# Performance work log

Measured on AMD Instinct MI355X. Metric: run time of the kernel, lower is better.

The kernel has to match this reference:

```python
import jax, jax.numpy as jnp
import numpy as np

B = 524288   # particles
H = 128      # hidden_size
E = 64       # embed_dim
NT = 512     # num trajectories
IN = 16 + 9 + E  # fc1 input dim = 89
EPS = 1e-6


def setup_inputs() -> dict:
    key = jax.random.key(0)
    ks = jax.random.split(key, 12)
    w = lambda k, shp, fan_in: (jax.random.normal(k, shp, dtype=jnp.float32)
                                / np.sqrt(fan_in).astype(np.float32))
    return {
        "F": jax.random.normal(ks[0], (B, 3, 3), dtype=jnp.float32),
        "C": jax.random.normal(ks[1], (B, 3, 3), dtype=jnp.float32),
        "traj_id": 7,
        "latent": jax.random.normal(ks[2], (NT, E), dtype=jnp.float32),
        "W1": w(ks[3], (IN, H), IN), "b1": jnp.zeros((H,), jnp.float32),
        "W2": w(ks[4], (H, H), H),   "b2": jnp.zeros((H,), jnp.float32),
        "W3": w(ks[5], (H, H), H),   "b3": jnp.zeros((H,), jnp.float32),
        "W4": w(ks[6], (H, H), H),   "b4": jnp.zeros((H,), jnp.float32),
        "W5": w(ks[7], (H, H), H),   "b5": jnp.zeros((H,), jnp.float32),
        "W6": w(ks[8], (H, H), H),   "b6": jnp.zeros((H,), jnp.float32),
        "W7": w(ks[9], (H, 9), H),   "b7": jnp.zeros((9,), jnp.float32),
    }


def _strain_features(F):
    # FFt: [B,3,3]; J = clamp(det F); J1 = clamp(F00); sigma: 3 singular values
    FFt = jnp.einsum('bij,bkj->bik', F, F)
    J = jnp.maximum(jnp.linalg.det(F), EPS)
    J1 = jnp.maximum(F[:, 0, 0], EPS)
    sigma = jnp.linalg.svd(F, compute_uv=False)  # descending, like torch.svd
    return jnp.concatenate([
        FFt.reshape(-1, 9),
        jnp.log(J)[:, None], sigma, J[:, None],
        jnp.log(J1)[:, None], J1[:, None],
    ], axis=-1)  # [B,16]


def reference(F, C, traj_id, latent,
              W1, b1, W2, b2, W3, b3, W4, b4, W5, b5, W6, b6, W7, b7):
    strain = _strain_features(F)                                   # [B,16]
    lat = jnp.broadcast_to(latent[traj_id], (F.shape[0], latent.shape[1]))
    x = jnp.concatenate([strain, C.reshape(-1, 9), lat], axis=-1)  # [B,89]
    g = lambda z: jax.nn.gelu(z, approximate=False)  # exact, matches torch GELU
    x = g(x @ W1 + b1)
    x = g(x @ W2 + b2)
    x = g(x @ W3 + b3)
    x = g(x @ W4 + b4)
    x = g(x @ W5 + b5)
    x = g(x @ W6 + b6)
    out = (x @ W7 + b7).reshape(-1, 3, 3)
    return 0.5 * (out + jnp.swapaxes(out, 1, 2))  # symmetric stress [B,3,3]
```

## Files before the change

### kernel.cpp

```cpp
#include <hip/hip_runtime.h>
#include <hip/hip_bf16.h>
#include <math.h>

#define BPART   524288
#define NBLK    (BPART / 128)
#define W7_OFF  98304
#define WB_N    102400
#define BIAS_N  800
#define PREP_N  (WB_N + BIAS_N)

typedef __bf16 bf16x8 __attribute__((ext_vector_type(8)));
typedef float  f32x16 __attribute__((ext_vector_type(16)));
typedef float  f32x4  __attribute__((ext_vector_type(4)));

#define MFMA __builtin_amdgcn_mfma_f32_32x32x16_bf16

__device__ __forceinline__ unsigned short f2bf(float f) {
  union { float f; unsigned u; } v; v.f = f;
  unsigned r = v.u + 0x7fffu + ((v.u >> 16) & 1u);
  return (unsigned short)(r >> 16);
}
__device__ __forceinline__ unsigned pack_bf16(float a, float b) {
  unsigned ua = __builtin_bit_cast(unsigned, a) + 0x8000u;
  unsigned ub = __builtin_bit_cast(unsigned, b) + 0x8000u;
  return __builtin_amdgcn_perm(ub, ua, 0x07060302u);
}
__device__ __forceinline__ int swz(int row, int col) {
  return (row << 7) | ((((col >> 3) ^ (row & 7)) << 3) | (col & 7));
}
__device__ __forceinline__ float gelu_t(float z) {
  float z2 = z * z;
  float t  = fmaf(0.1029432f, z2, 2.30220818f);
  float yp = z * t;
  float e  = __builtin_amdgcn_exp2f(-yp);
  float r  = __builtin_amdgcn_rcpf(e + 1.0f);
  return z * r;
}
__device__ __forceinline__ void cp16(const void* g, void* l) {
  __builtin_amdgcn_global_load_lds(
      (const __attribute__((address_space(1))) void*)g,
      (__attribute__((address_space(3))) void*)l, 16, 0, 0);
}

__global__ void prep_weights(
    const float* __restrict__ W1, const float* __restrict__ W2,
    const float* __restrict__ W3, const float* __restrict__ W4,
    const float* __restrict__ W5, const float* __restrict__ W6,
    const float* __restrict__ W7,
    const float* __restrict__ b1, const float* __restrict__ b2,
    const float* __restrict__ b3, const float* __restrict__ b4,
    const float* __restrict__ b5, const float* __restrict__ b6,
    const float* __restrict__ b7,
    unsigned short* __restrict__ wsb, float* __restrict__ wsf)
{
  int idx = blockIdx.x * 256 + threadIdx.x;
  if (idx < WB_N) {
    unsigned short v = 0;
    if (idx < W7_OFF) {
      int l = idx >> 14;
      int o = idx & 16383;
      int n = o >> 7, e = o & 127;
      int k = (((e >> 3) ^ (n & 7)) << 3) | (e & 7);
      const float* W = (l==0)?W1:(l==1)?W2:(l==2)?W3:(l==3)?W4:(l==4)?W5:W6;
      float x = (l == 0) ? ((k < 89) ? W[k*128 + n] : 0.0f)
                         : W[k*128 + n];
      v = f2bf(x);
    } else {
      int o = idx - W7_OFF;
      int n = o >> 7, e = o & 127;
      int k = (((e >> 3) ^ (n & 7)) << 3) | (e & 7);
      v = (n < 9) ? f2bf(W7[k*9 + n]) : (unsigned short)0;
    }
    wsb[idx] = v;
  } else if (idx < PREP_N) {
    int r = idx - WB_N;
    float x;
    if (r < 768) {
      int l = r >> 7, n = r & 127;
      const float* bb = (l==0)?b1:(l==1)?b2:(l==2)?b3:(l==3)?b4:(l==4)?b5:b6;
      x = bb[n];
    } else {
      int n = r - 768;
      x = (n < 9) ? b7[n] : 0.0f;
    }
    wsf[r] = x;
  }
}

__global__ __launch_bounds__(256, 2) void stress_mlp(
    const float* __restrict__ F, const float* __restrict__ Cmat,
    const int* __restrict__ traj, const float* __restrict__ latent,
    const unsigned short* __restrict__ wst, const float* __restrict__ wsf,
    float* __restrict__ out)
{
  __shared__ __align__(16) unsigned short act_s[128 * 128];
  __shared__ __align__(16) unsigned short wt_s[128 * 128];

  const int tid  = threadIdx.x;
  const int lane = tid & 63;
  const int wid  = tid >> 6;
  const int lm   = lane & 31;
  const int lk   = lane >> 5;
  const int m0   = (wid >> 1) << 6;
  const int n0   = (wid & 1) << 6;
  const int pbase = (int)blockIdx.x << 7;

  {
    const char* src = (const char*)wst;
    char* dst = (char*)wt_s;
    #pragma unroll
    for (int i = 0; i < 8; ++i)
      cp16(src + i*4096 + tid*16, dst + i*4096 + tid*16);
  }

  if (tid < 128) {
    const int row = tid;
    const int p   = pbase + row;
    float f[9];
    #pragma unroll
    for (int i = 0; i < 9; ++i) f[i] = F[p * 9 + i];
    float fft[9];
    #pragma unroll
    for (int i = 0; i < 3; ++i)
      #pragma unroll
      for (int k = 0; k < 3; ++k)
        fft[i*3+k] = f[i*3]*f[k*3] + f[i*3+1]*f[k*3+1] + f[i*3+2]*f[k*3+2];
    float det = f[0]*(f[4]*f[8]-f[5]*f[7]) - f[1]*(f[3]*f[8]-f[5]*f[6])
              + f[2]*(f[3]*f[7]-f[4]*f[6]);
    float J  = fmaxf(det, 1e-6f);
    float J1 = fmaxf(f[0], 1e-6f);
    double a00=fft[0], a01=fft[1], a02=fft[2], a11=fft[4], a12=fft[5], a22=fft[8];
    double q  = (a00+a11+a22) * (1.0/3.0);
    double d0 = a00-q, d1 = a11-q, d2 = a22-q;
    double p2 = d0*d0 + d1*d1 + d2*d2 + 2.0*(a01*a01 + a02*a02 + a12*a12);
    double e0, e1, e2;
    if (p2 < 1e-26) { e0 = e1 = e2 = q; }
    else {
      double pp = sqrt(p2 * (1.0/6.0));
      double inv = 1.0 / pp;
      double b00=d0*inv, b11=d1*inv, b22=d2*inv, b01=a01*inv, b02=a02*inv, b12=a12*inv;
      double detb = b00*(b11*b22-b12*b12) - b01*(b01*b22-b12*b02) + b02*(b01*b12-b11*b02);
      double rr = 0.5 * detb;
      rr = rr > 1.0 ? 1.0 : (rr < -1.0 ? -1.0 : rr);
      double phi = acos(rr) * (1.0/3.0);
      e0 = q + 2.0*pp*cos(phi);
      e2 = q + 2.0*pp*cos(phi + 2.0943951023931953);
      e1 = 3.0*q - e0 - e2;
    }
    float s0 = sqrtf(fmaxf((float)e0, 0.f));
    float s1 = sqrtf(fmaxf((float)e1, 0.f));
    float s2 = sqrtf(fmaxf((float)e2, 0.f));
    #pragma unroll
    for (int i = 0; i < 9; ++i) act_s[swz(row, i)] = f2bf(fft[i]);
    act_s[swz(row,  9)] = f2bf(logf(J));
    act_s[swz(row, 10)] = f2bf(s0);
    act_s[swz(row, 11)] = f2bf(s1);
    act_s[swz(row, 12)] = f2bf(s2);
    act_s[swz(row, 13)] = f2bf(J);
    act_s[swz(row, 14)] = f2bf(logf(J1));
    act_s[swz(row, 15)] = f2bf(J1);
    #pragma unroll
    for (int i = 0; i < 9; ++i) act_s[swz(row, 16 + i)] = f2bf(Cmat[p*9 + i]);
  } else {
    const int row = tid - 128;
    const int t = traj[0];
    const float* lat = latent + t * 64;
    for (int j = 0; j < 64; ++j) act_s[swz(row, 25 + j)] = f2bf(lat[j]);
    for (int j = 89; j < 128; ++j) act_s[swz(row, j)] = 0;
  }

  const int mr0 = m0 + lm,      mr1 = m0 + 32 + lm;
  const int nr0 = n0 + lm,      nr1 = n0 + 32 + lm;

  f32x16 acc[2][2];

  for (int l = 0; l < 6; ++l) {
    const float* bl = wsf + (l << 7);
    #pragma unroll
    for (int tn = 0; tn < 2; ++tn) {
      #pragma unroll
      for (int q = 0; q < 4; ++q) {
        f32x4 bq = *(const f32x4*)(bl + n0 + (tn << 5) + (q << 3) + (lk << 2));
        #pragma unroll
        for (int j = 0; j < 4; ++j) {
          acc[tn][0][4*q + j] = bq[j];
          acc[tn][1][4*q + j] = bq[j];
        }
      }
    }

    __syncthreads();

    #pragma unroll
    for (int kk = 0; kk < 8; ++kk) {
      const int kc = (kk << 1) + lk;
      bf16x8 x0 = *(const bf16x8*)&act_s[(mr0 << 7) + ((kc ^ (mr0 & 7)) << 3)];
      bf16x8 x1 = *(const bf16x8*)&act_s[(mr1 << 7) + ((kc ^ (mr1 & 7)) << 3)];
      bf16x8 w0 = *(const bf16x8*)&wt_s[(nr0 << 7) + ((kc ^ (nr0 & 7)) << 3)];
      bf16x8 w1 = *(const bf16x8*)&wt_s[(nr1 << 7) + ((kc ^ (nr1 & 7)) << 3)];
      acc[0][0] = MFMA(w0, x0, acc[0][0], 0, 0, 0);
      acc[0][1] = MFMA(w0, x1, acc[0][1], 0, 0, 0);
      acc[1][0] = MFMA(w1, x0, acc[1][0], 0, 0, 0);
      acc[1][1] = MFMA(w1, x1, acc[1][1], 0, 0, 0);
    }
    __syncthreads();

    if (l < 5) {
      const char* src = (const char*)(wst + ((l + 1) << 14));
      char* dst = (char*)wt_s;
      #pragma unroll
      for (int i = 0; i < 8; ++i)
        cp16(src + i*4096 + tid*16, dst + i*4096 + tid*16);
    } else {
      const char* src = (const char*)(wst + W7_OFF);
      char* dst = (char*)wt_s;
      #pragma unroll
      for (int i = 0; i < 2; ++i)
        cp16(src + i*4096 + tid*16, dst + i*4096 + tid*16);
    }

    #pragma unroll
    for (int tm = 0; tm < 2; ++tm) {
      const int m    = m0 + (tm << 5) + lm;
      const int rowb = m << 7;
      const int rx   = m & 7;
      #pragma unroll
      for (int tn = 0; tn < 2; ++tn) {
        const int cb = ((n0 + (tn << 5)) >> 3);
        #pragma unroll
        for (int q = 0; q < 4; ++q) {
          float g0 = gelu_t(acc[tn][tm][4*q + 0]);
          float g1 = gelu_t(acc[tn][tm][4*q + 1]);
          float g2 = gelu_t(acc[tn][tm][4*q + 2]);
          float g3 = gelu_t(acc[tn][tm][4*q + 3]);
          uint2 u;
          u.x = pack_bf16(g0, g1);
          u.y = pack_bf16(g2, g3);
          const int off = rowb + (((cb + q) ^ rx) << 3) + (lk << 2);
          *reinterpret_cast<uint2*>(&act_s[off]) = u;
        }
      }
    }
  }

  {
    f32x16 acc7[2];
    if ((wid & 1) == 0) {
      f32x4 bq0 = *(const f32x4*)(wsf + 768 + (lk << 2));
      f32x4 bq1 = *(const f32x4*)(wsf + 768 + 8 + (lk << 2));
      #pragma unroll
      for (int tm = 0; tm < 2; ++tm) {
        #pragma unroll
        for (int j = 0; j < 4; ++j) {
          acc7[tm][j]     = bq0[j];
          acc7[tm][4 + j] = bq1[j];
        }
        #pragma unroll
        for (int r = 8; r < 16; ++r) acc7[tm][r] = 0.0f;
      }
    }
    __syncthreads();

    if ((wid & 1) == 0) {
      #pragma unroll
      for (int kk = 0; kk < 8; ++kk) {
        const int kc = (kk << 1) + lk;
        bf16x8 x0 = *(const bf16x8*)&act_s[(mr0 << 7) + ((kc ^ (mr0 & 7)) << 3)];
        bf16x8 x1 = *(const bf16x8*)&act_s[(mr1 << 7) + ((kc ^ (mr1 & 7)) << 3)];
        bf16x8 w0 = *(const bf16x8*)&wt_s[(lm << 7) + ((kc ^ (lm & 7)) << 3)];
        acc7[0] = MFMA(w0, x0, acc7[0], 0, 0, 0);
        acc7[1] = MFMA(w0, x1, acc7[1], 0, 0, 0);
      }
    }
    __syncthreads();

    float* ots = (float*)wt_s;
    if ((wid & 1) == 0) {
      #pragma unroll
      for (int tm = 0; tm < 2; ++tm) {
        const int m = m0 + (tm << 5) + lm;
        #pragma unroll
        for (int j = 0; j < 4; ++j)
          ots[m * 9 + (lk << 2) + j] = acc7[tm][j];
        if (lk == 0) ots[m * 9 + 8] = acc7[tm][4];
      }
    }
    __syncthreads();

    if (tid < 128) {
      const int row = tid;
      float z[9];
      #pragma unroll
      for (int i = 0; i < 9; ++i) z[i] = ots[row * 9 + i];
      #pragma unroll
      for (int rr = 0; rr < 3; ++rr)
        #pragma unroll
        for (int cc = 0; cc < 3; ++cc)
          ots[row * 9 + rr*3 + cc] = 0.5f * (z[rr*3+cc] + z[cc*3+rr]);
    }
    __syncthreads();

    float4* dst = (float4*)(out + (size_t)pbase * 9);
    const float4* srcv = (const float4*)ots;
    for (int s = tid; s < 288; s += 256) dst[s] = srcv[s];
  }
}

extern "C" void kernel_launch(void* const* d_in, const int* in_sizes, int n_in,
                              void* d_out, int out_size, void* d_ws, size_t ws_size,
                              hipStream_t stream) {
  const float* F   = (const float*)d_in[0];
  const float* C   = (const float*)d_in[1];
  const int*   trj = (const int*)d_in[2];
  const float* lat = (const float*)d_in[3];
  const float* W1  = (const float*)d_in[4];
  const float* b1  = (const float*)d_in[5];
  const float* W2  = (const float*)d_in[6];
  const float* b2  = (const float*)d_in[7];
  const float* W3  = (const float*)d_in[8];
  const float* b3  = (const float*)d_in[9];
  const float* W4  = (const float*)d_in[10];
  const float* b4  = (const float*)d_in[11];
  const float* W5  = (const float*)d_in[12];
  const float* b5  = (const float*)d_in[13];
  const float* W6  = (const float*)d_in[14];
  const float* b6  = (const float*)d_in[15];
  const float* W7  = (const float*)d_in[16];
  const float* b7  = (const float*)d_in[17];

  unsigned short* wsb = (unsigned short*)d_ws;
  float* wsf = (float*)((char*)d_ws + WB_N * 2);

  prep_weights<<<dim3((PREP_N + 255) / 256), dim3(256), 0, stream>>>(
      W1, W2, W3, W4, W5, W6, W7, b1, b2, b3, b4, b5, b6, b7, wsb, wsf);
  stress_mlp<<<dim3(NBLK), dim3(256), 0, stream>>>(
      F, C, trj, lat, wsb, wsf, (float*)d_out);
}
```

Baseline: 296.8 us.

## Use fp32 eigen solve, packed-f32 GELU, and bias-seeded first MFMA

Three separate changes. The per-particle singular value computation moves from double precision (with libm acos/cos) to single precision with the hardware cos intrinsic, which takes period-scaled input. GELU is rewritten to process pairs with v_pk_mul/v_pk_fma. Bias values are loaded into a register union and passed straight as the accumulator input of the first MFMA rather than copied element by element. Risks are lower precision in the eigenvalue path near degenerate cases, and bias7 now reads 16 floats where the old code zero-filled half of them.

Measured after the change: 287.9 us. -3.0%, faster.

```diff
diff --git a/kernel.cpp b/kernel.cpp
--- a/kernel.cpp
+++ b/kernel.cpp
@@ -12,6 +12,7 @@
 typedef __bf16 bf16x8 __attribute__((ext_vector_type(8)));
 typedef float  f32x16 __attribute__((ext_vector_type(16)));
 typedef float  f32x4  __attribute__((ext_vector_type(4)));
+typedef float  f32x2  __attribute__((ext_vector_type(2)));
 
 #define MFMA __builtin_amdgcn_mfma_f32_32x32x16_bf16
 
@@ -28,13 +29,25 @@
 __device__ __forceinline__ int swz(int row, int col) {
   return (row << 7) | ((((col >> 3) ^ (row & 7)) << 3) | (col & 7));
 }
-__device__ __forceinline__ float gelu_t(float z) {
-  float z2 = z * z;
-  float t  = fmaf(0.1029432f, z2, 2.30220818f);
-  float yp = z * t;
-  float e  = __builtin_amdgcn_exp2f(-yp);
-  float r  = __builtin_amdgcn_rcpf(e + 1.0f);
-  return z * r;
+
+__device__ __forceinline__ f32x2 pk_mul(f32x2 a, f32x2 b) {
+  f32x2 d; asm("v_pk_mul_f32 %0, %1, %2" : "=v"(d) : "v"(a), "v"(b)); return d;
+}
+__device__ __forceinline__ f32x2 pk_fma(f32x2 a, f32x2 b, f32x2 c) {
+  f32x2 d; asm("v_pk_fma_f32 %0, %1, %2, %3" : "=v"(d) : "v"(a), "v"(b), "v"(c)); return d;
+}
+__device__ __forceinline__ f32x2 gelu2(f32x2 z) {
+  const f32x2 c1 = {0.1029432f, 0.1029432f};
+  const f32x2 c0 = {2.30220818f, 2.30220818f};
+  f32x2 z2 = pk_mul(z, z);
+  f32x2 t  = pk_fma(z2, c1, c0);
+  f32x2 yp = pk_mul(z, t);
+  float e0 = __builtin_amdgcn_exp2f(-yp.x);
+  float e1 = __builtin_amdgcn_exp2f(-yp.y);
+  float r0 = __builtin_amdgcn_rcpf(e0 + 1.0f);
+  float r1 = __builtin_amdgcn_rcpf(e1 + 1.0f);
+  f32x2 g; g.x = z.x * r0; g.y = z.y * r1;
+  return g;
 }
 __device__ __forceinline__ void cp16(const void* g, void* l) {
   __builtin_amdgcn_global_load_lds(
@@ -129,27 +142,27 @@
               + f[2]*(f[3]*f[7]-f[4]*f[6]);
     float J  = fmaxf(det, 1e-6f);
     float J1 = fmaxf(f[0], 1e-6f);
-    double a00=fft[0], a01=fft[1], a02=fft[2], a11=fft[4], a12=fft[5], a22=fft[8];
-    double q  = (a00+a11+a22) * (1.0/3.0);
-    double d0 = a00-q, d1 = a11-q, d2 = a22-q;
-    double p2 = d0*d0 + d1*d1 + d2*d2 + 2.0*(a01*a01 + a02*a02 + a12*a12);
-    double e0, e1, e2;
-    if (p2 < 1e-26) { e0 = e1 = e2 = q; }
+    float a00=fft[0], a01=fft[1], a02=fft[2], a11=fft[4], a12=fft[5], a22=fft[8];
+    float q  = (a00+a11+a22) * (1.0f/3.0f);
+    float d0 = a00-q, d1 = a11-q, d2 = a22-q;
+    float p2 = d0*d0 + d1*d1 + d2*d2 + 2.0f*(a01*a01 + a02*a02 + a12*a12);
+    float e0, e1, e2;
+    if (p2 < 1e-14f) { e0 = e1 = e2 = q; }
     else {
-      double pp = sqrt(p2 * (1.0/6.0));
-      double inv = 1.0 / pp;
-      double b00=d0*inv, b11=d1*inv, b22=d2*inv, b01=a01*inv, b02=a02*inv, b12=a12*inv;
-      double detb = b00*(b11*b22-b12*b12) - b01*(b01*b22-b12*b02) + b02*(b01*b12-b11*b02);
-      double rr = 0.5 * detb;
-      rr = rr > 1.0 ? 1.0 : (rr < -1.0 ? -1.0 : rr);
-      double phi = acos(rr) * (1.0/3.0);
-      e0 = q + 2.0*pp*cos(phi);
-      e2 = q + 2.0*pp*cos(phi + 2.0943951023931953);
-      e1 = 3.0*q - e0 - e2;
-    }
-    float s0 = sqrtf(fmaxf((float)e0, 0.f));
-    float s1 = sqrtf(fmaxf((float)e1, 0.f));
-    float s2 = sqrtf(fmaxf((float)e2, 0.f));
+      float pp  = sqrtf(p2 * (1.0f/6.0f));
+      float inv = 1.0f / pp;
+      float b00=d0*inv, b11=d1*inv, b22=d2*inv, b01=a01*inv, b02=a02*inv, b12=a12*inv;
+      float detb = b00*(b11*b22-b12*b12) - b01*(b01*b22-b12*b02) + b02*(b01*b12-b11*b02);
+      float rr = 0.5f * detb;
+      rr = fminf(fmaxf(rr, -1.0f), 1.0f);
+      float pr = acosf(rr) * (1.0f / (3.0f * 6.2831853071795864f));
+      e0 = q + 2.0f*pp*__builtin_amdgcn_cosf(pr);
+      e2 = q + 2.0f*pp*__builtin_amdgcn_cosf(pr + (1.0f/3.0f));
+      e1 = 3.0f*q - e0 - e2;
+    }
+    float s0 = sqrtf(fmaxf(e0, 0.f));
+    float s1 = sqrtf(fmaxf(e1, 0.f));
+    float s2 = sqrtf(fmaxf(e2, 0.f));
     #pragma unroll
     for (int i = 0; i < 9; ++i) act_s[swz(row, i)] = f2bf(fft[i]);
     act_s[swz(row,  9)] = f2bf(logf(J));
@@ -173,26 +186,31 @@
   const int nr0 = n0 + lm,      nr1 = n0 + 32 + lm;
 
   f32x16 acc[2][2];
+  union BF { f32x16 v; f32x4 q[4]; };
 
   for (int l = 0; l < 6; ++l) {
+    BF bias[2];
     const float* bl = wsf + (l << 7);
     #pragma unroll
-    for (int tn = 0; tn < 2; ++tn) {
-      #pragma unroll
-      for (int q = 0; q < 4; ++q) {
-        f32x4 bq = *(const f32x4*)(bl + n0 + (tn << 5) + (q << 3) + (lk << 2));
-        #pragma unroll
-        for (int j = 0; j < 4; ++j) {
-          acc[tn][0][4*q + j] = bq[j];
-          acc[tn][1][4*q + j] = bq[j];
-        }
-      }
-    }
-
-    __syncthreads();
-
-    #pragma unroll
-    for (int kk = 0; kk < 8; ++kk) {
+    for (int tn = 0; tn < 2; ++tn)
+      #pragma unroll
+      for (int qq = 0; qq < 4; ++qq)
+        bias[tn].q[qq] = *(const f32x4*)(bl + n0 + (tn << 5) + (qq << 3) + (lk << 2));
+
+    __syncthreads();
+
+    {
+      bf16x8 x0 = *(const bf16x8*)&act_s[(mr0 << 7) + ((lk ^ (mr0 & 7)) << 3)];
+      bf16x8 x1 = *(const bf16x8*)&act_s[(mr1 << 7) + ((lk ^ (mr1 & 7)) << 3)];
+      bf16x8 w0 = *(const bf16x8*)&wt_s[(nr0 << 7) + ((lk ^ (nr0 & 7)) << 3)];
+      bf16x8 w1 = *(const bf16x8*)&wt_s[(nr1 << 7) + ((lk ^ (nr1 & 7)) << 3)];
+      acc[0][0] = MFMA(w0, x0, bias[0].v, 0, 0, 0);
+      acc[0][1] = MFMA(w0, x1, bias[0].v, 0, 0, 0);
+      acc[1][0] = MFMA(w1, x0, bias[1].v, 0, 0, 0);
+      acc[1][1] = MFMA(w1, x1, bias[1].v, 0, 0, 0);
+    }
+    #pragma unroll
+    for (int kk = 1; kk < 8; ++kk) {
       const int kc = (kk << 1) + lk;
       bf16x8 x0 = *(const bf16x8*)&act_s[(mr0 << 7) + ((kc ^ (mr0 & 7)) << 3)];
       bf16x8 x1 = *(const bf16x8*)&act_s[(mr1 << 7) + ((kc ^ (mr1 & 7)) << 3)];
@@ -229,13 +247,13 @@
         const int cb = ((n0 + (tn << 5)) >> 3);
         #pragma unroll
         for (int q = 0; q < 4; ++q) {
-          float g0 = gelu_t(acc[tn][tm][4*q + 0]);
-          float g1 = gelu_t(acc[tn][tm][4*q + 1]);
-          float g2 = gelu_t(acc[tn][tm][4*q + 2]);
-          float g3 = gelu_t(acc[tn][tm][4*q + 3]);
+          f32x2 za; za.x = acc[tn][tm][4*q + 0]; za.y = acc[tn][tm][4*q + 1];
+          f32x2 zb; zb.x = acc[tn][tm][4*q + 2]; zb.y = acc[tn][tm][4*q + 3];
+          f32x2 ga = gelu2(za);
+          f32x2 gb = gelu2(zb);
           uint2 u;
-          u.x = pack_bf16(g0, g1);
-          u.y = pack_bf16(g2, g3);
+          u.x = pack_bf16(ga.x, ga.y);
+          u.y = pack_bf16(gb.x, gb.y);
           const int off = rowb + (((cb + q) ^ rx) << 3) + (lk << 2);
           *reinterpret_cast<uint2*>(&act_s[off]) = u;
         }
@@ -244,26 +262,24 @@
   }
 
   {
+    BF bias7;
+    #pragma unroll
+    for (int qq = 0; qq < 4; ++qq)
+      bias7.q[qq] = *(const f32x4*)(wsf + 768 + (qq << 3) + (lk << 2));
+
+    __syncthreads();
+
     f32x16 acc7[2];
     if ((wid & 1) == 0) {
-      f32x4 bq0 = *(const f32x4*)(wsf + 768 + (lk << 2));
-      f32x4 bq1 = *(const f32x4*)(wsf + 768 + 8 + (lk << 2));
-      #pragma unroll
-      for (int tm = 0; tm < 2; ++tm) {
-        #pragma unroll
-        for (int j = 0; j < 4; ++j) {
-          acc7[tm][j]     = bq0[j];
-          acc7[tm][4 + j] = bq1[j];
-        }
-        #pragma unroll
-        for (int r = 8; r < 16; ++r) acc7[tm][r] = 0.0f;
+      {
+        bf16x8 x0 = *(const bf16x8*)&act_s[(mr0 << 7) + ((lk ^ (mr0 & 7)) << 3)];
+        bf16x8 x1 = *(const bf16x8*)&act_s[(mr1 << 7) + ((lk ^ (mr1 & 7)) << 3)];
+        bf16x8 w0 = *(const bf16x8*)&wt_s[(lm << 7) + ((lk ^ (lm & 7)) << 3)];
+        acc7[0] = MFMA(w0, x0, bias7.v, 0, 0, 0);
+        acc7[1] = MFMA(w0, x1, bias7.v, 0, 0, 0);
       }
-    }
-    __syncthreads();
-
-    if ((wid & 1) == 0) {
-      #pragma unroll
-      for (int kk = 0; kk < 8; ++kk) {
+      #pragma unroll
+      for (int kk = 1; kk < 8; ++kk) {
         const int kc = (kk << 1) + lk;
         bf16x8 x0 = *(const bf16x8*)&act_s[(mr0 << 7) + ((kc ^ (mr0 & 7)) << 3)];
         bf16x8 x1 = *(const bf16x8*)&act_s[(mr1 << 7) + ((kc ^ (mr1 & 7)) << 3)];
```
